# Kernel tuning notes

Hardware: AMD Instinct MI355X
Metric: run time of the kernel (lower is better)

The kernel has to match this reference:

```python
import jax, jax.numpy as jnp
import numpy as np

B, N_PROP = 2, 512
C_FEAT, FH, FW = 256, 200, 200
NUM_CLASSES, NUM_STAGES = 81, 3
POOL, SR, SCALE = 7, 2, 0.25
IMG_H, IMG_W = 800.0, 800.0
FC_DIM = 1024
IN_DIM = C_FEAT * POOL * POOL
STDS = ((0.1, 0.1, 0.2, 0.2), (0.05, 0.05, 0.1, 0.1), (0.033, 0.033, 0.067, 0.067))
CLIP_VAL = float(np.log(1000.0 / 16))
SCORE_T, NMS_T, DETS, PRE_NMS = 0.05, 0.5, 100, 2048


def bilinear(f, y, x):
    # f: [C,H,W]; y,x: [M] sample coords (torchvision roi_align bilinear rules)
    H, W = f.shape[1], f.shape[2]
    valid = (y > -1.0) & (y < H) & (x > -1.0) & (x < W)
    y = jnp.clip(y, 0.0, H - 1.0)
    x = jnp.clip(x, 0.0, W - 1.0)
    y0 = jnp.floor(y).astype(jnp.int32)
    x0 = jnp.floor(x).astype(jnp.int32)
    y1 = jnp.minimum(y0 + 1, H - 1)
    x1 = jnp.minimum(x0 + 1, W - 1)
    ly, lx = y - y0, x - x0
    hy, hx = 1.0 - ly, 1.0 - lx
    v = (hy * hx) * f[:, y0, x0] + (hy * lx) * f[:, y0, x1] \
      + (ly * hx) * f[:, y1, x0] + (ly * lx) * f[:, y1, x1]
    return v * valid  # [C,M]


def roi_align(f, rois):
    # f: [C,H,W], rois: [N,4] image coords -> [N,C,POOL,POOL]
    b = rois * SCALE
    x1, y1, x2, y2 = b[:, 0], b[:, 1], b[:, 2], b[:, 3]
    rw = jnp.maximum(x2 - x1, 1.0)
    rh = jnp.maximum(y2 - y1, 1.0)
    bw, bh = rw / POOL, rh / POOL
    p = jnp.arange(POOL, dtype=f.dtype)
    s = (jnp.arange(SR, dtype=f.dtype) + 0.5) / SR
    gy = y1[:, None, None] + (p[None, :, None] + s[None, None, :]) * bh[:, None, None]  # [N,P,SR]
    gx = x1[:, None, None] + (p[None, :, None] + s[None, None, :]) * bw[:, None, None]
    n = rois.shape[0]
    yy = jnp.broadcast_to(gy[:, :, :, None, None], (n, POOL, SR, POOL, SR))
    xx = jnp.broadcast_to(gx[:, None, None, :, :], (n, POOL, SR, POOL, SR))
    vals = bilinear(f, yy.reshape(-1), xx.reshape(-1))  # [C, N*P*SR*P*SR]
    vals = vals.reshape(f.shape[0], n, POOL, SR, POOL, SR).mean(axis=(3, 5))
    return vals.transpose(1, 0, 2, 3)


def decode_clip(props, deltas, stds):
    px1, py1, px2, py2 = props[:, 0], props[:, 1], props[:, 2], props[:, 3]
    pw = jnp.maximum(px2 - px1, 1e-6)
    ph = jnp.maximum(py2 - py1, 1e-6)
    px = px1 + 0.5 * pw
    py = py1 + 0.5 * ph
    wx, wy, ww, wh = stds
    dx = deltas[:, 0] * wx
    dy = deltas[:, 1] * wy
    dw = jnp.minimum(deltas[:, 2] * ww, CLIP_VAL)
    dh = jnp.minimum(deltas[:, 3] * wh, CLIP_VAL)
    gx = dx * pw + px
    gy = dy * ph + py
    gw = jnp.exp(dw) * pw
    gh = jnp.exp(dh) * ph
    return jnp.stack([jnp.clip(gx - 0.5 * gw, 0.0, IMG_W),
                      jnp.clip(gy - 0.5 * gh, 0.0, IMG_H),
                      jnp.clip(gx + 0.5 * gw, 0.0, IMG_W),
                      jnp.clip(gy + 0.5 * gh, 0.0, IMG_H)], axis=1)


def box_iou(a, b):
    area_a = (a[:, 2] - a[:, 0]) * (a[:, 3] - a[:, 1])
    area_b = (b[:, 2] - b[:, 0]) * (b[:, 3] - b[:, 1])
    lt = jnp.maximum(a[:, None, :2], b[None, :, :2])
    rb = jnp.minimum(a[:, None, 2:], b[None, :, 2:])
    wh = jnp.maximum(rb - lt, 0.0)
    inter = wh[..., 0] * wh[..., 1]
    return inter / (area_a[:, None] + area_b[None, :] - inter + 1e-12)


def postprocess(boxes, probs):
    # boxes [N,4], probs [N,NUM_CLASSES] -> fixed-size padded detections
    n = boxes.shape[0]
    ws = boxes[:, 2] - boxes[:, 0]
    hs = boxes[:, 3] - boxes[:, 1]
    ok = (ws >= 1.0) & (hs >= 1.0)  # remove_small_boxes(min_size=1.0)
    fg = probs[:, 1:]               # drop background (class 0)
    sc = jnp.where((fg > SCORE_T) & ok[:, None], fg, -1.0).reshape(-1)  # [N*(C-1)]
    labels = jnp.broadcast_to(jnp.arange(1, NUM_CLASSES, dtype=jnp.int32)[None, :],
                              (n, NUM_CLASSES - 1)).reshape(-1)
    bflat = jnp.broadcast_to(boxes[:, None, :], (n, NUM_CLASSES - 1, 4)).reshape(-1, 4)
    vals, idx = jax.lax.top_k(sc, PRE_NMS)  # fixed-size candidate cap, sorted desc
    bsel = bflat[idx]
    lsel = labels[idx]
    # batched_nms trick: offset boxes per label so classes never overlap
    off = bsel + (lsel.astype(bsel.dtype) * (jnp.max(bsel) + 1.0))[:, None]
    iou = box_iou(off, off)
    valid = vals > 0.0
    ar = jnp.arange(PRE_NMS)
    def body(i, keep):
        sup = (iou[i] > NMS_T) & keep[i]
        return keep & ~(sup & (ar > i))
    keep = jax.lax.fori_loop(0, PRE_NMS, body, valid)
    order = jnp.argsort(jnp.where(keep, ar, PRE_NMS + ar))[:DETS]  # kept first, score order
    kv = keep[order]
    out_boxes = jnp.where(kv[:, None], bsel[order], 0.0)
    out_scores = jnp.where(kv, vals[order], 0.0)
    out_labels = jnp.where(kv, lsel[order], 0)
    return out_boxes, out_scores, out_labels


def cascade_forward(features, proposals, W1, b1, W2, b2, Wc, bc, Wr, br):
    cur = proposals  # [B,N,4]
    logits = None
    for s in range(NUM_STAGES):
        pooled = jax.vmap(roi_align)(features, cur)  # [B,N,C,P,P]
        x = pooled.reshape(B * N_PROP, IN_DIM)
        h = jax.nn.relu(x @ W1[s] + b1[s])
        h = jax.nn.relu(h @ W2[s] + b2[s])
        logits = h @ Wc[s] + bc[s]
        deltas = (h @ Wr[s] + br[s]).reshape(B, N_PROP, 4)
        stds = STDS[s]
        cur = jax.vmap(lambda p, d: decode_clip(p, d, stds))(cur, deltas)
    probs = jax.nn.softmax(logits, axis=-1).reshape(B, N_PROP, NUM_CLASSES)
    return jax.vmap(postprocess)(cur, probs)


def setup_inputs() -> dict:
    key = jax.random.key(0)
    ks = jax.random.split(key, 12)
    features = jax.random.normal(ks[0], (B, C_FEAT, FH, FW), jnp.float32)
    cx = jax.random.uniform(ks[1], (B, N_PROP), minval=0.0, maxval=IMG_W)
    cy = jax.random.uniform(ks[2], (B, N_PROP), minval=0.0, maxval=IMG_H)
    w = jax.random.uniform(ks[3], (B, N_PROP), minval=16.0, maxval=256.0)
    h = jax.random.uniform(ks[4], (B, N_PROP), minval=16.0, maxval=256.0)
    proposals = jnp.stack([jnp.clip(cx - w / 2, 0.0, IMG_W), jnp.clip(cy - h / 2, 0.0, IMG_H),
                           jnp.clip(cx + w / 2, 0.0, IMG_W), jnp.clip(cy + h / 2, 0.0, IMG_H)],
                          axis=-1)
    def lin(k, fan_in, shape):
        return jax.random.normal(k, shape, jnp.float32) / np.sqrt(fan_in).astype(np.float32)
    W1 = lin(ks[5], IN_DIM, (NUM_STAGES, IN_DIM, FC_DIM))
    W2 = lin(ks[6], FC_DIM, (NUM_STAGES, FC_DIM, FC_DIM))
    Wc = lin(ks[7], FC_DIM, (NUM_STAGES, FC_DIM, NUM_CLASSES))
    Wr = lin(ks[8], FC_DIM, (NUM_STAGES, FC_DIM, 4)) * 0.5
    b1 = jnp.zeros((NUM_STAGES, FC_DIM), jnp.float32)
    b2 = jnp.zeros((NUM_STAGES, FC_DIM), jnp.float32)
    bc = jnp.zeros((NUM_STAGES, NUM_CLASSES), jnp.float32)
    br = jnp.zeros((NUM_STAGES, 4), jnp.float32)
    return {"features": features, "proposals": proposals, "W1": W1, "b1": b1,
            "W2": W2, "b2": b2, "Wc": Wc, "bc": bc, "Wr": Wr, "br": br}


def reference(features, proposals, W1, b1, W2, b2, Wc, bc, Wr, br):
    return cascade_forward(features, proposals, W1, b1, W2, b2, Wc, bc, Wr, br)
```

## Files before the change

### kernel.cpp

```cpp
#include <hip/hip_runtime.h>
#include <float.h>
#include <math.h>

#define NB 2
#define NPROP 512
#define NROI 1024
#define CFEAT 256
#define FH 200
#define FW 200
#define HWSZ 40000
#define INDIM 12544
#define FCD 1024
#define NCLS 81
#define NCAND 40960
#define CAP 4096
#define NSEL 2048
#define DETS 100
#define CLIPV 4.135166556742356f

#define KKT1 392
#define KKT2 32
#define SPLITK 8

typedef __attribute__((ext_vector_type(8))) short short8v;
typedef __attribute__((ext_vector_type(8))) unsigned short ushort8v;
typedef __attribute__((ext_vector_type(4))) float float4v;

__device__ __forceinline__ unsigned short f2bf(float x) {
    unsigned u = __float_as_uint(x);
    unsigned r = (u + 0x7fffu + ((u >> 16) & 1u)) >> 16;
    return (unsigned short)r;
}
__device__ __forceinline__ float bf2f(unsigned short b) {
    return __uint_as_float(((unsigned)b) << 16);
}
__device__ __forceinline__ void split3(float x, unsigned short& h, unsigned short& m, unsigned short& l) {
    h = f2bf(x);
    float r1 = x - bf2f(h);
    m = f2bf(r1);
    float r2 = r1 - bf2f(m);
    l = f2bf(r2);
}

__device__ __forceinline__ void gload_lds16(const void* g, void* l) {
    __builtin_amdgcn_global_load_lds((const __attribute__((address_space(1))) unsigned int*)g,
                                     (__attribute__((address_space(3))) unsigned int*)l, 16, 0, 0);
}

__device__ __forceinline__ int swz8k(int o) {
    return o ^ ((((o >> 6) ^ (o >> 8)) & 3) << 4);
}

__global__ void zero_ints_k(int* p, int n) {
    int i = blockIdx.x * blockDim.x + threadIdx.x;
    if (i < n) p[i] = 0;
}

__global__ __launch_bounds__(256) void transpose_k(const float* __restrict__ in, float* __restrict__ out) {
    __shared__ float tile[32][33];
    int b = blockIdx.z;
    int hw0 = blockIdx.x * 32;
    int c0 = blockIdx.y * 32;
    int tx = threadIdx.x;
    int ty = threadIdx.y;
#pragma unroll
    for (int i = 0; i < 32; i += 8)
        tile[ty + i][tx] = in[((size_t)(b * CFEAT + c0 + ty + i)) * HWSZ + hw0 + tx];
    __syncthreads();
#pragma unroll
    for (int i = 0; i < 32; i += 8)
        out[((size_t)b * HWSZ + hw0 + ty + i) * CFEAT + c0 + tx] = tile[tx][ty + i];
}

template<bool TRANS>
__device__ __forceinline__ float bil_sample(const float* __restrict__ feat, int b, int c,
                                            float yy, float xx) {
    bool valid = (yy > -1.f) && (yy < (float)FH) && (xx > -1.f) && (xx < (float)FW);
    float yc = fminf(fmaxf(yy, 0.f), (float)(FH - 1));
    float xc = fminf(fmaxf(xx, 0.f), (float)(FW - 1));
    int y0 = (int)floorf(yc), x0 = (int)floorf(xc);
    int y1i = min(y0 + 1, FH - 1), x1i = min(x0 + 1, FW - 1);
    float ly = yc - (float)y0, lx = xc - (float)x0;
    float hy = 1.f - ly, hx = 1.f - lx;
    float v00, v01, v10, v11;
    if (TRANS) {
        const float* base = feat + (size_t)b * HWSZ * CFEAT;
        v00 = base[((size_t)(y0 * FW + x0)) * CFEAT + c];
        v01 = base[((size_t)(y0 * FW + x1i)) * CFEAT + c];
        v10 = base[((size_t)(y1i * FW + x0)) * CFEAT + c];
        v11 = base[((size_t)(y1i * FW + x1i)) * CFEAT + c];
    } else {
        const float* base = feat + ((size_t)(b * CFEAT + c)) * HWSZ;
        v00 = base[y0 * FW + x0];
        v01 = base[y0 * FW + x1i];
        v10 = base[y1i * FW + x0];
        v11 = base[y1i * FW + x1i];
    }
    float v = hy * hx * v00 + hy * lx * v01 + ly * hx * v10 + ly * lx * v11;
    return valid ? v : 0.f;
}

template<bool TRANS>
__global__ __launch_bounds__(256) void roi_k(const float* __restrict__ feat,
                                             const float* __restrict__ boxes,
                                             float* __restrict__ xout) {
    int pp = blockIdx.x, r = blockIdx.y, c = threadIdx.x;
    int b = r >> 9;
    const float* bx = boxes + (size_t)r * 4;
    float x1 = bx[0] * 0.25f, y1 = bx[1] * 0.25f, x2 = bx[2] * 0.25f, y2 = bx[3] * 0.25f;
    float rw = fmaxf(x2 - x1, 1.0f), rh = fmaxf(y2 - y1, 1.0f);
    float bw = rw / 7.0f, bh = rh / 7.0f;
    int py = pp / 7, px = pp % 7;
    float acc = 0.f;
#pragma unroll
    for (int sy = 0; sy < 2; ++sy)
#pragma unroll
        for (int sx = 0; sx < 2; ++sx)
            acc += bil_sample<TRANS>(feat, b, c,
                                     y1 + ((float)py + 0.25f + 0.5f * (float)sy) * bh,
                                     x1 + ((float)px + 0.25f + 0.5f * (float)sx) * bw);
    xout[(size_t)r * INDIM + pp * 256 + c] = acc * 0.25f;
}

__global__ __launch_bounds__(256) void roi_split4_k(const float* __restrict__ feat,
                                                    const float* __restrict__ boxes,
                                                    unsigned short* __restrict__ Ap) {
    int tid = threadIdx.x;
    int g = tid >> 7;
    int binhalf = (tid >> 6) & 1;
    int cl = tid & 63;
    int r = blockIdx.x * 2 + g;
    int b = r >> 9;
    const float* bx = boxes + (size_t)r * 4;
    float x1 = bx[0] * 0.25f, y1 = bx[1] * 0.25f, x2 = bx[2] * 0.25f, y2 = bx[3] * 0.25f;
    float rw = fmaxf(x2 - x1, 1.0f), rh = fmaxf(y2 - y1, 1.0f);
    float bw = rw / 7.0f, bh = rh / 7.0f;
    int mt = r >> 7, rr = r & 127;
    size_t pstr = (size_t)8 * KKT1 * 4096;
    const float* base = feat + (size_t)b * HWSZ * CFEAT;
    for (int pp = binhalf; pp < 49; pp += 2) {
        int py = pp / 7, px = pp % 7;
        float ax = 0.f, ay = 0.f, az = 0.f, aw = 0.f;
#pragma unroll
        for (int sy = 0; sy < 2; ++sy) {
#pragma unroll
            for (int sx = 0; sx < 2; ++sx) {
                float yy = y1 + ((float)py + 0.25f + 0.5f * (float)sy) * bh;
                float xx = x1 + ((float)px + 0.25f + 0.5f * (float)sx) * bw;
                bool valid = (yy > -1.f) && (yy < (float)FH) && (xx > -1.f) && (xx < (float)FW);
                float yc = fminf(fmaxf(yy, 0.f), (float)(FH - 1));
                float xc = fminf(fmaxf(xx, 0.f), (float)(FW - 1));
                int y0 = (int)floorf(yc), x0 = (int)floorf(xc);
                int y1i = min(y0 + 1, FH - 1), x1i = min(x0 + 1, FW - 1);
                float ly = yc - (float)y0, lx = xc - (float)x0;
                float hy = 1.f - ly, hx = 1.f - lx;
                float w00 = hy * hx, w01 = hy * lx, w10 = ly * hx, w11 = ly * lx;
                if (!valid) { w00 = w01 = w10 = w11 = 0.f; }
                float4 v00 = ((const float4*)(base + (size_t)(y0 * FW + x0) * CFEAT))[cl];
                float4 v01 = ((const float4*)(base + (size_t)(y0 * FW + x1i) * CFEAT))[cl];
                float4 v10 = ((const float4*)(base + (size_t)(y1i * FW + x0) * CFEAT))[cl];
                float4 v11 = ((const float4*)(base + (size_t)(y1i * FW + x1i) * CFEAT))[cl];
                ax += w00 * v00.x + w01 * v01.x + w10 * v10.x + w11 * v11.x;
                ay += w00 * v00.y + w01 * v01.y + w10 * v10.y + w11 * v11.y;
                az += w00 * v00.z + w01 * v01.z + w10 * v10.z + w11 * v11.z;
                aw += w00 * v00.w + w01 * v01.w + w10 * v10.w + w11 * v11.w;
            }
        }
        ax *= 0.25f; ay *= 0.25f; az *= 0.25f; aw *= 0.25f;
        ushort4 h4, m4, l4;
        split3(ax, h4.x, m4.x, l4.x);
        split3(ay, h4.y, m4.y, l4.y);
        split3(az, h4.z, m4.z, l4.z);
        split3(aw, h4.w, m4.w, l4.w);
        int k0 = pp * 256 + cl * 4;
        int kk = k0 >> 5;
        size_t tile = ((size_t)mt * KKT1 + kk) * 4096 + rr * 32 + (k0 & 31);
        *(ushort4*)&Ap[tile] = h4;
        *(ushort4*)&Ap[tile + pstr] = m4;
        *(ushort4*)&Ap[tile + 2 * pstr] = l4;
    }
}

template<bool PERM>
__global__ __launch_bounds__(256) void wsplit_k(const float* __restrict__ W,
                                                unsigned short* __restrict__ out, int kkT) {
    __shared__ float tf[32][132];
    int nt = blockIdx.x, kk = blockIdx.y;
    int t = threadIdx.x;
    int kloc = t >> 3;
    int f4 = t & 7;
    int krow;
    if (PERM) krow = ((kk & 7) * 32 + kloc) * 49 + (kk >> 3);
    else krow = kk * 32 + kloc;
    const float* src = W + (size_t)krow * 1024 + nt * 128;
#pragma unroll
    for (int q = 0; q < 4; ++q) {
        float4 v = *(const float4*)(src + (f4 + q * 8) * 4);
        *(float4*)&tf[kloc][(f4 + q * 8) * 4] = v;
    }
    __syncthreads();
    int r = t >> 1;
    size_t tileBase = ((size_t)nt * kkT + kk) * 4096;
    size_t pstr = (size_t)8 * kkT * 4096;
#pragma unroll
    for (int cc = 0; cc < 2; ++cc) {
        int c = (t & 1) * 2 + cc;
        ushort8v hv, mv, lv;
#pragma unroll
        for (int e = 0; e < 8; ++e) {
            unsigned short h, m, l;
            split3(tf[c * 8 + e][r], h, m, l);
            hv[e] = h; mv[e] = m; lv[e] = l;
        }
        size_t o = tileBase + r * 32 + c * 8;
        *(ushort8v*)&out[o] = hv;
        *(ushort8v*)&out[o + pstr] = mv;
        *(ushort8v*)&out[o + 2 * pstr] = lv;
    }
}

__global__ __launch_bounds__(256) void wsplit_head_k(const float* __restrict__ Wc,
                                                     const float* __restrict__ Wr,
                                                     unsigned short* __restrict__ out) {
    int kk = blockIdx.x, t = threadIdx.x;
    int r = t >> 1;
    int k0 = (t & 1) * 16;
    size_t pstr = (size_t)KKT2 * 4096;
    for (int e = 0; e < 16; ++e) {
        int k = k0 + e;
        int krow = kk * 32 + k;
        float v = 0.f;
        if (r < 81) v = Wc[(size_t)krow * 81 + r];
        else if (r < 85) v = Wr[(size_t)krow * 4 + (r - 81)];
        unsigned short h, m, l;
        split3(v, h, m, l);
        size_t o = (size_t)kk * 4096 + r * 32 + k;
        out[o] = h;
        out[o + pstr] = m;
        out[o + 2 * pstr] = l;
    }
}

#define TERM16(AF) { _Pragma("unroll") for (int i = 0; i < 4; ++i) _Pragma("unroll") \
    for (int j = 0; j < 4; ++j) acc[i][j] = __builtin_amdgcn_mfma_f32_16x16x32_bf16(AF[i], bf[j], acc[i][j], 0, 0, 0); }

__global__ __launch_bounds__(256) void gemm_mfma_k(const unsigned short* __restrict__ Ap,
                                                   const unsigned short* __restrict__ Bp,
                                                   float* __restrict__ partial,
                                                   int kkT, int kkPer, int NT, int N) {
    __shared__ unsigned short sA[3][4096];
    __shared__ unsigned short sB[3][4096];
    int tid = threadIdx.x;
    int phys = blockIdx.x;
    int logical = (phys & 7) * (gridDim.x >> 3) + (phys >> 3);
    int tpc = 8 * NT;
    int xy = logical % tpc;
    int ck = logical / tpc;
    int mt = xy & 7, nt = xy >> 3;
    int kk0 = ck * kkPer;
    size_t pstrA = (size_t)8 * kkT * 4096 * 2;
    size_t pstrB = (size_t)NT * kkT * 4096 * 2;
    const char* aBase = (const char*)(Ap + (size_t)mt * kkT * 4096);
    const char* bBase = (const char*)(Bp + (size_t)nt * kkT * 4096);

    float4v acc[4][4];
#pragma unroll
    for (int i = 0; i < 4; ++i)
#pragma unroll
        for (int j = 0; j < 4; ++j) acc[i][j] = (float4v){0.f, 0.f, 0.f, 0.f};

    int lane = tid & 63, wv = tid >> 6;
    int wr = wv >> 1, wc = wv & 1;
    int ln = lane & 15;
    int q = lane >> 4;
    int qs = (q ^ (ln ^ (ln >> 2))) & 3;
    int aoffE = (wr * 64 + ln) * 32 + qs * 8;
    int boffE = (wc * 64 + ln) * 32 + qs * 8;

    int o0 = tid * 16;
    int o1 = o0 + 4096;
    int s0 = swz8k(o0);
    int s1 = swz8k(o1);

    for (int kk = kk0; kk < kk0 + kkPer; ++kk) {
        const char* at = aBase + (size_t)kk * 8192;
        const char* bt = bBase + (size_t)kk * 8192;
#pragma unroll
        for (int p = 0; p < 3; ++p) {
            gload_lds16(at + (size_t)p * pstrA + s0, (char*)sA[p] + o0);
            gload_lds16(at + (size_t)p * pstrA + s1, (char*)sA[p] + o1);
            gload_lds16(bt + (size_t)p * pstrB + s0, (char*)sB[p] + o0);
            gload_lds16(bt + (size_t)p * pstrB + s1, (char*)sB[p] + o1);
        }
        __syncthreads();
        short8v af[3][4];
#pragma unroll
        for (int p = 0; p < 3; ++p)
#pragma unroll
            for (int f = 0; f < 4; ++f)
                af[p][f] = *(const short8v*)&sA[p][aoffE + f * 512];
        short8v bf[4];
#pragma unroll
        for (int f = 0; f < 4; ++f) bf[f] = *(const short8v*)&sB[0][boffE + f * 512];
        TERM16(af[0]); TERM16(af[1]); TERM16(af[2]);
#pragma unroll
        for (int f = 0; f < 4; ++f) bf[f] = *(const short8v*)&sB[1][boffE + f * 512];
        TERM16(af[0]); TERM16(af[1]);
#pragma unroll
        for (int f = 0; f < 4; ++f) bf[f] = *(const short8v*)&sB[2][boffE + f * 512];
        TERM16(af[0]);
        __syncthreads();
    }
    float* outp = partial + (size_t)ck * 1024 * N;
    int row0 = mt * 128 + wr * 64 + (lane >> 4) * 4;
    int col = nt * 128 + wc * 64 + ln;
#pragma unroll
    for (int i = 0; i < 4; ++i)
#pragma unroll
        for (int j = 0; j < 4; ++j)
#pragma unroll
            for (int qq = 0; qq < 4; ++qq)
                outp[(size_t)(row0 + i * 16 + qq) * N + col + j * 16] = acc[i][j][qq];
}

template<int NS>
__global__ void reduce8_k(const float* __restrict__ partial, const float* __restrict__ bias,
                          unsigned short* __restrict__ planes) {
    int i = blockIdx.x * 256 + threadIdx.x;
    float s = 0.f;
#pragma unroll
    for (int c = 0; c < NS; ++c) s += partial[((size_t)c << 20) + i];
    s += bias[i & 1023];
    s = fmaxf(s, 0.f);
    int m = i >> 10, n = i & 1023;
    int mt = m >> 7, rr = m & 127, kk = n >> 5;
    unsigned short h, mm_, l;
    split3(s, h, mm_, l);
    size_t tile = ((size_t)mt * KKT2 + kk) * 4096 + rr * 32 + (n & 31);
    size_t pstr = (size_t)8 * KKT2 * 4096;
    planes[tile] = h;
    planes[tile + pstr] = mm_;
    planes[tile + 2 * pstr] = l;
}

__global__ void head_fin_k(const float* __restrict__ partial, const float* __restrict__ bc,
                           const float* __restrict__ br, float* __restrict__ logits,
                           float* __restrict__ deltas, int write_logits) {
    int idx = blockIdx.x * 256 + threadIdx.x;
    if (idx >= 1024 * 85) return;
    int m = idx / 85, col = idx - m * 85;
    float s = 0.f;
#pragma unroll
    for (int c = 0; c < 8; ++c) s += partial[(size_t)c * 131072 + m * 128 + col];
    if (col < 81) {
        if (write_logits) logits[(size_t)m * NCLS + col] = s + bc[col];
    } else {
        deltas[(size_t)m * 4 + (col - 81)] = s + br[col - 81];
    }
}

template<bool PERM>
__global__ __launch_bounds__(256) void gemm_k(const float* __restrict__ A,
                                              const float* __restrict__ Bm,
                                              float* __restrict__ partial,
                                              int K_total, int Kchunk) {
    const int M = 1024, N = 1024;
    __shared__ float As[2][16][128];
    __shared__ float Bs[2][16][64];
    int tid = threadIdx.x;
    int mb = blockIdx.x & 7;
    int nb = blockIdx.x >> 3;
    int ck = blockIdx.y;
    int k0 = ck * Kchunk;
    int am = tid >> 1;
    int ak = (tid & 1) * 8;
    int bk = tid >> 4;
    int bn = (tid & 15) * 4;
    int ty = tid >> 4, tx = tid & 15;
    const float* Aptr = A + (size_t)(mb * 128 + am) * K_total + k0 + ak;

    float acc[8][4];
#pragma unroll
    for (int i = 0; i < 8; ++i)
#pragma unroll
        for (int j = 0; j < 4; ++j) acc[i][j] = 0.f;

    auto bRowPtr = [&](int kk) -> const float* {
        int row = PERM ? ((kk & 255) * 49 + (kk >> 8)) : kk;
        return Bm + (size_t)row * N + nb * 64 + bn;
    };

    int T = Kchunk / 16;
    float4 a0 = *(const float4*)(Aptr);
    float4 a1 = *(const float4*)(Aptr + 4);
    float4 b0 = *(const float4*)bRowPtr(k0 + bk);
    As[0][ak + 0][am] = a0.x; As[0][ak + 1][am] = a0.y; As[0][ak + 2][am] = a0.z; As[0][ak + 3][am] = a0.w;
    As[0][ak + 4][am] = a1.x; As[0][ak + 5][am] = a1.y; As[0][ak + 6][am] = a1.z; As[0][ak + 7][am] = a1.w;
    *(float4*)&Bs[0][bk][bn] = b0;
    __syncthreads();

    int p = 0;
    for (int t = 0; t < T; ++t) {
        if (t + 1 < T) {
            a0 = *(const float4*)(Aptr + (t + 1) * 16);
            a1 = *(const float4*)(Aptr + (t + 1) * 16 + 4);
            b0 = *(const float4*)bRowPtr(k0 + (t + 1) * 16 + bk);
        }
#pragma unroll
        for (int k = 0; k < 16; ++k) {
            float4 av0 = *(const float4*)&As[p][k][ty * 8];
            float4 av1 = *(const float4*)&As[p][k][ty * 8 + 4];
            float4 bv = *(const float4*)&Bs[p][k][tx * 4];
            float ar[8] = {av0.x, av0.y, av0.z, av0.w, av1.x, av1.y, av1.z, av1.w};
            float br_[4] = {bv.x, bv.y, bv.z, bv.w};
#pragma unroll
            for (int i = 0; i < 8; ++i)
#pragma unroll
                for (int j = 0; j < 4; ++j) acc[i][j] = fmaf(ar[i], br_[j], acc[i][j]);
        }
        if (t + 1 < T) {
            __syncthreads();
            int qb = 1 - p;
            As[qb][ak + 0][am] = a0.x; As[qb][ak + 1][am] = a0.y; As[qb][ak + 2][am] = a0.z; As[qb][ak + 3][am] = a0.w;
            As[qb][ak + 4][am] = a1.x; As[qb][ak + 5][am] = a1.y; As[qb][ak + 6][am] = a1.z; As[qb][ak + 7][am] = a1.w;
            *(float4*)&Bs[qb][bk][bn] = b0;
            __syncthreads();
            p = qb;
        }
    }
    float* out = partial + ((size_t)ck * M + mb * 128 + ty * 8) * N + nb * 64 + tx * 4;
#pragma unroll
    for (int i = 0; i < 8; ++i) {
        float4 v = make_float4(acc[i][0], acc[i][1], acc[i][2], acc[i][3]);
        *(float4*)(out + (size_t)i * N) = v;
    }
}

__global__ void reduce4_k(const float* __restrict__ partial, const float* __restrict__ bias,
                          float* __restrict__ out) {
    const int MN = 1024 * 1024;
    int i = blockIdx.x * 256 + threadIdx.x;
    if (i >= MN) return;
    float s = partial[i] + partial[(size_t)MN + i] + partial[(size_t)2 * MN + i] + partial[(size_t)3 * MN + i];
    s += bias[i & 1023];
    out[i] = fmaxf(s, 0.f);
}

__global__ __launch_bounds__(128) void head_k(const float* __restrict__ h,
                                              const float* __restrict__ Wc, const float* __restrict__ bc,
                                              const float* __restrict__ Wr, const float* __restrict__ br,
                                              float* __restrict__ logits, float* __restrict__ deltas,
                                              int write_logits) {
    __shared__ float hs[1024];
    int m = blockIdx.x;
    int tid = threadIdx.x;
    const float4* hp = (const float4*)(h + (size_t)m * 1024);
    ((float4*)hs)[tid] = hp[tid];
    ((float4*)hs)[tid + 128] = hp[tid + 128];
    __syncthreads();
    int j = tid;
    if (j < 85) {
        bool is_cls = j < 81;
        const float* Wp = is_cls ? Wc : Wr;
        int stride = is_cls ? 81 : 4;
        int col = is_cls ? j : j - 81;
        float s0 = 0.f, s1 = 0.f, s2 = 0.f, s3 = 0.f;
        for (int k = 0; k < 1024; k += 4) {
            s0 = fmaf(hs[k + 0], Wp[(k + 0) * stride + col], s0);
            s1 = fmaf(hs[k + 1], Wp[(k + 1) * stride + col], s1);
            s2 = fmaf(hs[k + 2], Wp[(k + 2) * stride + col], s2);
            s3 = fmaf(hs[k + 3], Wp[(k + 3) * stride + col], s3);
        }
        float s = (s0 + s1) + (s2 + s3);
        if (is_cls) {
            if (write_logits) logits[(size_t)m * NCLS + col] = s + bc[col];
        } else {
            deltas[(size_t)m * 4 + col] = s + br[col];
        }
    }
}

__global__ void decode_k(const float* __restrict__ prev, const float* __restrict__ deltas,
                         float* __restrict__ nxt, float wx, float wy, float ww, float wh) {
    int r = blockIdx.x * 256 + threadIdx.x;
    if (r >= NROI) return;
    const float* p = prev + (size_t)r * 4;
    const float* d = deltas + (size_t)r * 4;
    float px1 = p[0], py1 = p[1], px2 = p[2], py2 = p[3];
    float pw = fmaxf(px2 - px1, 1e-6f), ph = fmaxf(py2 - py1, 1e-6f);
    float pcx = px1 + 0.5f * pw, pcy = py1 + 0.5f * ph;
    float dx = d[0] * wx, dy = d[1] * wy;
    float dw = fminf(d[2] * ww, CLIPV);
    float dh = fminf(d[3] * wh, CLIPV);
    float gx = dx * pw + pcx, gy = dy * ph + pcy;
    float gw = expf(dw) * pw, gh = expf(dh) * ph;
    nxt[(size_t)r * 4 + 0] = fminf(fmaxf(gx - 0.5f * gw, 0.f), 800.f);
    nxt[(size_t)r * 4 + 1] = fminf(fmaxf(gy - 0.5f * gh, 0.f), 800.f);
    nxt[(size_t)r * 4 + 2] = fminf(fmaxf(gx + 0.5f * gw, 0.f), 800.f);
    nxt[(size_t)r * 4 + 3] = fminf(fmaxf(gy + 0.5f * gh, 0.f), 800.f);
}

__global__ __launch_bounds__(128) void softmax_k(const float* __restrict__ logits, float* __restrict__ probs) {
    __shared__ float red[128];
    int m = blockIdx.x;
    int tid = threadIdx.x;
    float v = (tid < NCLS) ? logits[(size_t)m * NCLS + tid] : -FLT_MAX;
    red[tid] = v;
    __syncthreads();
    for (int o = 64; o; o >>= 1) {
        if (tid < o) red[tid] = fmaxf(red[tid], red[tid + o]);
        __syncthreads();
    }
    float mx = red[0];
    __syncthreads();
    float e = (tid < NCLS) ? expf(v - mx) : 0.f;
    red[tid] = e;
    __syncthreads();
    for (int o = 64; o; o >>= 1) {
        if (tid < o) red[tid] += red[tid + o];
        __syncthreads();
    }
    float s = red[0];
    if (tid < NCLS) probs[(size_t)m * NCLS + tid] = e / s;
}

__global__ void build_scores_k(const float* __restrict__ probs, const float* __restrict__ boxes,
                               float* __restrict__ sc, int* __restrict__ vcount) {
    int f = blockIdx.x * 256 + threadIdx.x;
    if (f >= NB * NCAND) return;
    int b = f / NCAND, ff = f % NCAND;
    int rr = ff / 80, cls = ff % 80 + 1;
    int row = b * NPROP + rr;
    const float* bx = boxes + (size_t)row * 4;
    bool ok = (bx[2] - bx[0] >= 1.f) && (bx[3] - bx[1] >= 1.f);
    float p = probs[(size_t)row * NCLS + cls];
    float s = (p > 0.05f && ok) ? p : -1.0f;
    sc[f] = s;
    if (s > 0.f) atomicAdd(&vcount[b], 1);
}

__global__ __launch_bounds__(1024) void find_pivot_k(const float* __restrict__ sc,
                                                     const int* __restrict__ vcount,
                                                     float* __restrict__ pivot) {
    int b = blockIdx.x;
    const float* s = sc + (size_t)b * NCAND;
    __shared__ int tot;
    int V = vcount[b];
    if (V <= CAP) {
        if (threadIdx.x == 0) pivot[b] = 0.f;
        return;
    }
    unsigned u = 0;
    for (int bit = 30; bit >= 0; --bit) {
        unsigned cand = u | (1u << bit);
        float cf = __uint_as_float(cand);
        if (threadIdx.x == 0) tot = 0;
        __syncthreads();
        int cnt = 0;
        for (int i = threadIdx.x; i < NCAND; i += 1024) cnt += (s[i] >= cf) ? 1 : 0;
        for (int o = 32; o; o >>= 1) cnt += __shfl_down(cnt, o);
        if ((threadIdx.x & 63) == 0) atomicAdd(&tot, cnt);
        __syncthreads();
        if (tot >= NSEL) u = cand;
        __syncthreads();
    }
    if (threadIdx.x == 0) pivot[b] = __uint_as_float(u);
}

__global__ void compact_k(const float* __restrict__ sc, const float* __restrict__ pivot,
                          float* __restrict__ ckey, int* __restrict__ cidx, int* __restrict__ ccount) {
    int f = blockIdx.x * 256 + threadIdx.x;
    if (f >= NB * NCAND) return;
    int b = f / NCAND, ff = f % NCAND;
    float s = sc[f];
    float pv = pivot[b];
    if (s > 0.f && s >= pv) {
        int slot = atomicAdd(&ccount[b], 1);
        if (slot < CAP) {
            ckey[(size_t)b * CAP + slot] = s;
            cidx[(size_t)b * CAP + slot] = ff;
        }
    }
}

__global__ __launch_bounds__(1024) void sort_select_k(const float* __restrict__ ckey,
                                                      const int* __restrict__ cidx,
                                                      const int* __restrict__ ccount,
                                                      const float* __restrict__ boxes,
                                                      float* __restrict__ selb, float* __restrict__ seloff,
                                                      float* __restrict__ selsc, int* __restrict__ sellab,
                                                      unsigned long long* __restrict__ vmask) {
    int b = blockIdx.x;
    __shared__ float ks[CAP];
    __shared__ int is[CAP];
    __shared__ float rmax[1024];
    int cnt = min(ccount[b], CAP);
    for (int i = threadIdx.x; i < CAP; i += 1024) {
        if (i < cnt) {
            ks[i] = ckey[(size_t)b * CAP + i];
            is[i] = cidx[(size_t)b * CAP + i];
        } else {
            ks[i] = -FLT_MAX;
            is[i] = 0x7FFFFFFF;
        }
    }
    __syncthreads();
    for (int k = 2; k <= CAP; k <<= 1) {
        for (int j = k >> 1; j > 0; j >>= 1) {
            for (int t = threadIdx.x; t < CAP; t += 1024) {
                int l = t ^ j;
                if (l > t) {
                    bool up = ((t & k) == 0);
                    float a = ks[t], bb = ks[l];
                    int ia = is[t], ib = is[l];
                    bool a_first = (a > bb) || (a == bb && ia < ib);
                    bool doswap = up ? !a_first : a_first;
                    if (doswap) {
                        ks[t] = bb; ks[l] = a;
                        is[t] = ib; is[l] = ia;
                    }
                }
            }
            __syncthreads();
        }
    }
    float lm = -FLT_MAX;
    for (int i = threadIdx.x; i < NSEL; i += 1024) {
        if (ks[i] > 0.f) {
            const float* bb = boxes + (size_t)(b * NPROP + is[i] / 80) * 4;
            lm = fmaxf(lm, fmaxf(fmaxf(bb[0], bb[1]), fmaxf(bb[2], bb[3])));
        }
    }
    rmax[threadIdx.x] = lm;
    __syncthreads();
    for (int o = 512; o; o >>= 1) {
        if (threadIdx.x < o) rmax[threadIdx.x] = fmaxf(rmax[threadIdx.x], rmax[threadIdx.x + o]);
        __syncthreads();
    }
    float maxb = (rmax[0] > -FLT_MAX) ? rmax[0] : 0.f;
    __syncthreads();
    for (int pass = 0; pass < 2; ++pass) {
        int i = pass * 1024 + threadIdx.x;
        bool v = ks[i] > 0.f;
        int idx = is[i];
        int rr = idx / 80;
        int cls = idx % 80 + 1;
        float b0 = 0.f, b1 = 0.f, b2 = 0.f, b3 = 0.f, offv = 0.f;
        if (v) {
            const float* bb = boxes + (size_t)(b * NPROP + rr) * 4;
            b0 = bb[0]; b1 = bb[1]; b2 = bb[2]; b3 = bb[3];
            offv = (maxb + 1.f) * (float)cls;
        }
        float* sb = selb + ((size_t)b * NSEL + i) * 4;
        sb[0] = b0; sb[1] = b1; sb[2] = b2; sb[3] = b3;
        float* so = seloff + ((size_t)b * NSEL + i) * 4;
        so[0] = b0 + offv; so[1] = b1 + offv; so[2] = b2 + offv; so[3] = b3 + offv;
        selsc[(size_t)b * NSEL + i] = v ? ks[i] : 0.f;
        sellab[(size_t)b * NSEL + i] = cls;
        unsigned long long m = __ballot(v);
        if ((threadIdx.x & 63) == 0) vmask[b * 32 + pass * 16 + (threadIdx.x >> 6)] = m;
    }
}

__global__ __launch_bounds__(256) void sup_k(const float* __restrict__ seloff,
                                             const float* __restrict__ selsc,
                                             unsigned long long* __restrict__ sup) {
    int b = blockIdx.y;
    int wave = threadIdx.x >> 6;
    int lane = threadIdx.x & 63;
    int pair = blockIdx.x * 4 + wave;
    int i = pair >> 5;
    int w = pair & 31;
    int j = w * 64 + lane;
    unsigned long long m = 0;
    if (w >= (i >> 6) && selsc[(size_t)b * NSEL + i] > 0.f) {
        const float* oi = seloff + ((size_t)b * NSEL + i) * 4;
        const float* oj = seloff + ((size_t)b * NSEL + j) * 4;
        float ax1 = oi[0], ay1 = oi[1], ax2 = oi[2], ay2 = oi[3];
        float bx1 = oj[0], by1 = oj[1], bx2 = oj[2], by2 = oj[3];
        float areaA = (ax2 - ax1) * (ay2 - ay1);
        float areaB = (bx2 - bx1) * (by2 - by1);
        float ltx = fmaxf(ax1, bx1), lty = fmaxf(ay1, by1);
        float rbx = fminf(ax2, bx2), rby = fminf(ay2, by2);
        float iw = fmaxf(rbx - ltx, 0.f), ih = fmaxf(rby - lty, 0.f);
        float inter = iw * ih;
        float iou = inter / (areaA + areaB - inter + 1e-12f);
        m = __ballot(iou > 0.5f);
    }
    if (lane == 0) sup[((size_t)b * NSEL + i) * 32 + w] = m;
}

__global__ __launch_bounds__(256) void nms_scan_k(const unsigned long long* __restrict__ vmask,
                                                  const unsigned long long* __restrict__ sup,
                                                  const float* __restrict__ selb,
                                                  const float* __restrict__ selsc,
                                                  const int* __restrict__ sellab,
                                                  float* __restrict__ out) {
    int b = blockIdx.x;
    __shared__ unsigned long long keepw[32];
    __shared__ int pref[33];
    int tid = threadIdx.x;
    if (tid < 64) {
        int lane = tid;
        unsigned long long kw = (lane < 32) ? vmask[b * 32 + lane] : 0ull;
        const unsigned long long* srow = sup + (size_t)b * NSEL * 32 + (lane & 31);
        unsigned long long pre[16];
#pragma unroll
        for (int d = 0; d < 16; ++d)
            pre[d] = (lane < 32) ? srow[(size_t)d * 32] : 0ull;
        for (int i0 = 0; i0 < NSEL; i0 += 16) {
#pragma unroll
            for (int d = 0; d < 16; ++d) {
                int i = i0 + d;
                unsigned long long row = pre[d];
                int nf = i + 16;
                pre[d] = (lane < 32 && nf < NSEL) ? srow[(size_t)nf * 32] : 0ull;
                int wi = i >> 6;
                unsigned long long wv = __shfl(kw, wi);
                if ((wv >> (i & 63)) & 1ull) {
                    if (lane < 32) {
                        unsigned long long mask;
                        if (lane > wi) mask = ~0ull;
                        else if (lane == wi) mask = ((i & 63) == 63) ? 0ull : (~0ull << ((i & 63) + 1));
                        else mask = 0ull;
                        kw &= ~(row & mask);
                    }
                }
            }
        }
        if (lane < 32) keepw[lane] = kw;
    }
    __syncthreads();
    if (tid == 0) {
        int s = 0;
        for (int w = 0; w < 32; ++w) { pref[w] = s; s += __popcll(keepw[w]); }
        pref[32] = s;
    }
    __syncthreads();
    for (int i = tid; i < 600; i += 256) {
        if (i < 400) out[b * 400 + i] = 0.f;
        else if (i < 500) out[800 + b * 100 + (i - 400)] = 0.f;
        else out[1000 + b * 100 + (i - 500)] = 0.f;
    }
    __syncthreads();
    for (int e = tid; e < NSEL; e += 256) {
        int w = e >> 6;
        unsigned long long kw = keepw[w];
        if ((kw >> (e & 63)) & 1ull) {
            int rank = pref[w] + __popcll(kw & ((1ull << (e & 63)) - 1ull));
            if (rank < DETS) {
                const float* sb = selb + ((size_t)b * NSEL + e) * 4;
                out[b * 400 + rank * 4 + 0] = sb[0];
                out[b * 400 + rank * 4 + 1] = sb[1];
                out[b * 400 + rank * 4 + 2] = sb[2];
                out[b * 400 + rank * 4 + 3] = sb[3];
                out[800 + b * 100 + rank] = selsc[(size_t)b * NSEL + e];
                out[1000 + b * 100 + rank] = (float)sellab[(size_t)b * NSEL + e];
            }
        }
    }
}

extern "C" void kernel_launch(void* const* d_in, const int* in_sizes, int n_in,
                              void* d_out, int out_size, void* d_ws, size_t ws_size,
                              hipStream_t stream) {
    const float* features = (const float*)d_in[0];
    const float* proposals = (const float*)d_in[1];
    const float* W1 = (const float*)d_in[2];
    const float* b1 = (const float*)d_in[3];
    const float* W2 = (const float*)d_in[4];
    const float* b2 = (const float*)d_in[5];
    const float* Wc = (const float*)d_in[6];
    const float* bc = (const float*)d_in[7];
    const float* Wr = (const float*)d_in[8];
    const float* br = (const float*)d_in[9];

    char* ws = (char*)d_ws;
    size_t off = 0;
    auto alloc = [&](size_t bytes) -> void* {
        void* p = ws + off;
        off += (bytes + 255) & ~(size_t)255;
        return p;
    };

    float* logits = (float*)alloc((size_t)NROI * NCLS * 4);
    float* probs = (float*)alloc((size_t)NROI * NCLS * 4);
    float* deltas = (float*)alloc((size_t)NROI * 4 * 4);
    float* cur1 = (float*)alloc((size_t)NROI * 4 * 4);
    float* cur2 = (float*)alloc((size_t)NROI * 4 * 4);
    float* cur3 = (float*)alloc((size_t)NROI * 4 * 4);
    float* sc = (float*)alloc((size_t)NB * NCAND * 4);
    float* ckey = (float*)alloc((size_t)NB * CAP * 4);
    int* cidx = (int*)alloc((size_t)NB * CAP * 4);
    int* counters = (int*)alloc(256);
    float* pivot = (float*)(counters + 4);
    float* selb = (float*)alloc((size_t)NB * NSEL * 4 * 4);
    float* seloff = (float*)alloc((size_t)NB * NSEL * 4 * 4);
    float* selsc = (float*)alloc((size_t)NB * NSEL * 4);
    int* sellab = (int*)alloc((size_t)NB * NSEL * 4);
    unsigned long long* vmask = (unsigned long long*)alloc((size_t)NB * 32 * 8);
    unsigned long long* sup = (unsigned long long*)alloc((size_t)NB * NSEL * 32 * 8);

    const float stds[3][4] = {{0.1f, 0.1f, 0.2f, 0.2f},
                              {0.05f, 0.05f, 0.1f, 0.1f},
                              {0.033f, 0.033f, 0.067f, 0.067f}};
    float* curbufs[3] = {cur1, cur2, cur3};
    const float* curp = proposals;

    size_t planes1 = (size_t)3 * 8 * KKT1 * 4096 * 2;
    size_t planes2 = (size_t)3 * 8 * KKT2 * 4096 * 2;
    size_t planesH = (size_t)3 * 1 * KKT2 * 4096 * 2;
    size_t mfma_need = planes1 * 2 + planes2 * 3 + planesH +
                       (size_t)SPLITK * (1 << 20) * 4 +
                       (size_t)NB * HWSZ * CFEAT * 4 + 65536;

    zero_ints_k<<<1, 64, 0, stream>>>(counters, 4);

    if (off + mfma_need <= ws_size) {
        unsigned short* Ap1 = (unsigned short*)alloc(planes1);
        unsigned short* Bp1 = (unsigned short*)alloc(planes1);
        unsigned short* h1p = (unsigned short*)alloc(planes2);
        unsigned short* W2Tp = (unsigned short*)alloc(planes2);
        unsigned short* h2p = (unsigned short*)alloc(planes2);
        unsigned short* Whp = (unsigned short*)alloc(planesH);
        float* partial = (float*)alloc((size_t)SPLITK * (1 << 20) * 4);
        float* featT = (float*)alloc((size_t)NB * HWSZ * CFEAT * 4);

        transpose_k<<<dim3(1250, 8, 2), dim3(32, 8), 0, stream>>>(features, featT);

        for (int s = 0; s < 3; ++s) {
            roi_split4_k<<<dim3(NROI / 2), 256, 0, stream>>>(featT, curp, Ap1);
            wsplit_k<true><<<dim3(8, KKT1), 256, 0, stream>>>(W1 + (size_t)s * INDIM * FCD, Bp1, KKT1);
            gemm_mfma_k<<<dim3(64 * SPLITK), 256, 0, stream>>>(Ap1, Bp1, partial, KKT1, KKT1 / SPLITK, 8, 1024);
            reduce8_k<SPLITK><<<4096, 256, 0, stream>>>(partial, b1 + s * FCD, h1p);
            wsplit_k<false><<<dim3(8, KKT2), 256, 0, stream>>>(W2 + (size_t)s * FCD * FCD, W2Tp, KKT2);
            gemm_mfma_k<<<dim3(512), 256, 0, stream>>>(h1p, W2Tp, partial, KKT2, 4, 8, 1024);
            reduce8_k<8><<<4096, 256, 0, stream>>>(partial, b2 + s * FCD, h2p);
            wsplit_head_k<<<dim3(KKT2), 256, 0, stream>>>(Wc + (size_t)s * FCD * NCLS,
                                                          Wr + (size_t)s * FCD * 4, Whp);
            gemm_mfma_k<<<dim3(64), 256, 0, stream>>>(h2p, Whp, partial, KKT2, 4, 1, 128);
            head_fin_k<<<dim3(340), 256, 0, stream>>>(partial, bc + s * NCLS, br + s * 4,
                                                      logits, deltas, (s == 2) ? 1 : 0);
            decode_k<<<4, 256, 0, stream>>>(curp, deltas, curbufs[s],
                                            stds[s][0], stds[s][1], stds[s][2], stds[s][3]);
            curp = curbufs[s];
        }
    } else {
        float* x = (float*)alloc((size_t)NROI * INDIM * 4);
        float* partial = (float*)alloc((size_t)4 * 1024 * 1024 * 4);
        float* h1 = (float*)alloc((size_t)NROI * FCD * 4);
        float* h2 = (float*)alloc((size_t)NROI * FCD * 4);
        float* featT = (float*)alloc((size_t)NB * HWSZ * CFEAT * 4);
        bool use_trans = (off <= ws_size);

        if (use_trans)
            transpose_k<<<dim3(1250, 8, 2), dim3(32, 8), 0, stream>>>(features, featT);

        for (int s = 0; s < 3; ++s) {
            if (use_trans)
                roi_k<true><<<dim3(49, 1024), 256, 0, stream>>>(featT, curp, x);
            else
                roi_k<false><<<dim3(49, 1024), 256, 0, stream>>>(features, curp, x);
            gemm_k<true><<<dim3(128, 4), 256, 0, stream>>>(x, W1 + (size_t)s * INDIM * FCD, partial, INDIM, 3136);
            reduce4_k<<<4096, 256, 0, stream>>>(partial, b1 + s * FCD, h1);
            gemm_k<false><<<dim3(128, 4), 256, 0, stream>>>(h1, W2 + (size_t)s * FCD * FCD, partial, FCD, 256);
            reduce4_k<<<4096, 256, 0, stream>>>(partial, b2 + s * FCD, h2);
            head_k<<<1024, 128, 0, stream>>>(h2, Wc + (size_t)s * FCD * NCLS, bc + s * NCLS,
                                             Wr + (size_t)s * FCD * 4, br + s * 4,
                                             logits, deltas, (s == 2) ? 1 : 0);
            decode_k<<<4, 256, 0, stream>>>(curp, deltas, curbufs[s],
                                            stds[s][0], stds[s][1], stds[s][2], stds[s][3]);
            curp = curbufs[s];
        }
    }

    softmax_k<<<1024, 128, 0, stream>>>(logits, probs);
    build_scores_k<<<320, 256, 0, stream>>>(probs, curp, sc, counters);
    find_pivot_k<<<2, 1024, 0, stream>>>(sc, counters, pivot);
    compact_k<<<320, 256, 0, stream>>>(sc, pivot, ckey, cidx, counters + 2);
    sort_select_k<<<2, 1024, 0, stream>>>(ckey, cidx, counters + 2, curp, selb, seloff, selsc, sellab, vmask);
    sup_k<<<dim3(16384, 2), 256, 0, stream>>>(seloff, selsc, sup);
    nms_scan_k<<<2, 256, 0, stream>>>(vmask, sup, selb, selsc, sellab, (float*)d_out);
}
```

Measured before the change: 1.279 ms.

## Restructure NMS scan into word-blocked resolution with early exit

The sequential greedy NMS scan, which handled 2048 rows one at a time with a shuffle and mask per row, becomes a per-64-bit-word scheme. The diagonal block is resolved inside registers using shuffles. The kept rows' suppression masks are then OR-reduced across the wave and applied to later words in one step. The scan stops once at least DETS boxes are kept, which skips the remaining words. The early break leaves later keep words unsuppressed. Output must therefore take only the first DETS kept boxes in order for results to stay correct.

```diff
diff --git a/kernel.cpp b/kernel.cpp
--- a/kernel.cpp
+++ b/kernel.cpp
@@ -703,29 +703,43 @@
     if (tid < 64) {
         int lane = tid;
         unsigned long long kw = (lane < 32) ? vmask[b * 32 + lane] : 0ull;
-        const unsigned long long* srow = sup + (size_t)b * NSEL * 32 + (lane & 31);
-        unsigned long long pre[16];
-#pragma unroll
-        for (int d = 0; d < 16; ++d)
-            pre[d] = (lane < 32) ? srow[(size_t)d * 32] : 0ull;
-        for (int i0 = 0; i0 < NSEL; i0 += 16) {
-#pragma unroll
-            for (int d = 0; d < 16; ++d) {
-                int i = i0 + d;
-                unsigned long long row = pre[d];
-                int nf = i + 16;
-                pre[d] = (lane < 32 && nf < NSEL) ? srow[(size_t)nf * 32] : 0ull;
-                int wi = i >> 6;
-                unsigned long long wv = __shfl(kw, wi);
-                if ((wv >> (i & 63)) & 1ull) {
-                    if (lane < 32) {
-                        unsigned long long mask;
-                        if (lane > wi) mask = ~0ull;
-                        else if (lane == wi) mask = ((i & 63) == 63) ? 0ull : (~0ull << ((i & 63) + 1));
-                        else mask = 0ull;
-                        kw &= ~(row & mask);
-                    }
+        const unsigned long long* supB = sup + (size_t)b * NSEL * 32;
+        int kept = 0;
+        for (int w = 0; w < 32; ++w) {
+            unsigned long long cur = __shfl(kw, w);
+            if (cur) {
+                unsigned long long R = supB[(size_t)(w * 64 + lane) * 32 + w];
+                for (int b0 = 0; b0 < 64; b0 += 8) {
+                    unsigned long long r0 = __shfl(R, b0 + 0);
+                    unsigned long long r1 = __shfl(R, b0 + 1);
+                    unsigned long long r2 = __shfl(R, b0 + 2);
+                    unsigned long long r3 = __shfl(R, b0 + 3);
+                    unsigned long long r4 = __shfl(R, b0 + 4);
+                    unsigned long long r5 = __shfl(R, b0 + 5);
+                    unsigned long long r6 = __shfl(R, b0 + 6);
+                    unsigned long long r7 = __shfl(R, b0 + 7);
+                    unsigned long long hi;
+#define NMS_STEP(rr_, dd_) { int bb = b0 + dd_; \
+                    hi = (bb == 63) ? 0ull : (~0ull << (bb + 1)); \
+                    cur &= ~((0ull - ((cur >> bb) & 1ull)) & rr_ & hi); }
+                    NMS_STEP(r0, 0) NMS_STEP(r1, 1) NMS_STEP(r2, 2) NMS_STEP(r3, 3)
+                    NMS_STEP(r4, 4) NMS_STEP(r5, 5) NMS_STEP(r6, 6) NMS_STEP(r7, 7)
+#undef NMS_STEP
                 }
+                kept += __popcll(cur);
+                if (lane == w) kw = cur;
+                if (kept >= DETS) break;
+                int v = lane & 31;
+                int h = lane >> 5;
+                unsigned long long acc = 0;
+                const unsigned long long* rowb = supB + (size_t)(w * 64 + h) * 32 + v;
+#pragma unroll 8
+                for (int t = 0; t < 32; ++t) {
+                    unsigned long long msk = 0ull - ((cur >> (h + 2 * t)) & 1ull);
+                    acc |= rowb[(size_t)(2 * t) * 32] & msk;
+                }
+                acc |= __shfl_xor(acc, 32);
+                if (lane < 32 && lane > w) kw &= ~acc;
             }
         }
         if (lane < 32) keepw[lane] = kw;
```

New measurement: 1.083 ms. 1.18x faster.
